# Optimization experiments

Hardware: AMD Instinct MI355X
Metric: run time of the kernel (lower is better)

## Reference

```python
import jax, jax.numpy as jnp
import numpy as np

LATENT = 64
HEADS = 4
N_A, N_B = 1024, 1024


def setup_inputs() -> dict:
    key = jax.random.key(0)
    ks = jax.random.split(key, 10)
    L = LATENT
    return {
        "rho_real": jax.random.normal(ks[0], (N_A, N_B), dtype=jnp.float32),
        "rho_imag": jax.random.normal(ks[1], (N_A, N_B), dtype=jnp.float32),
        "l_A": jax.random.randint(ks[2], (N_A,), 0, 3),
        "l_B": jax.random.randint(ks[3], (N_B,), 0, 3),
        "Z_A": 6,
        "Z_B": 8,
        # block_encoder: Linear(2, 64) -> SiLU -> Linear(64, latent_dim)
        "W1": jax.random.normal(ks[4], (64, 2), dtype=jnp.float32) * 0.5,
        "b1": jnp.zeros((64,), dtype=jnp.float32),
        "W2": jax.random.normal(ks[5], (L, 64), dtype=jnp.float32) * 0.1,
        "b2": jnp.zeros((L,), dtype=jnp.float32),
        # learned pooling query (1, latent_dim)
        "query": jax.random.normal(ks[6], (1, L), dtype=jnp.float32),
        # nn.MultiheadAttention packed in-projection and out-projection
        "in_proj_w": jax.random.normal(ks[7], (3 * L, L), dtype=jnp.float32) * 0.1,
        "in_proj_b": jnp.zeros((3 * L,), dtype=jnp.float32),
        "out_proj_w": jax.random.normal(ks[8], (L, L), dtype=jnp.float32) * 0.1,
        "out_proj_b": jnp.zeros((L,), dtype=jnp.float32),
    }


def reference(rho_real, rho_imag, l_A, l_B, Z_A, Z_B,
              W1, b1, W2, b2, query, in_proj_w, in_proj_b,
              out_proj_w, out_proj_b):
    L = query.shape[-1]
    H = HEADS
    hd = L // H
    # Batched equivalent of the per-(i,j) loop: all n_A*n_B elements at once.
    x = jnp.stack([rho_real.reshape(-1), rho_imag.reshape(-1)], axis=-1)  # [N, 2]
    h = jax.nn.silu(x @ W1.T + b1) @ W2.T + b2                            # [N, L]
    # MultiheadAttention with single query (batch=1, tgt_len=1, src_len=N)
    Wq, Wk, Wv = in_proj_w[:L], in_proj_w[L:2 * L], in_proj_w[2 * L:]
    bq, bk, bv = in_proj_b[:L], in_proj_b[L:2 * L], in_proj_b[2 * L:]
    q = (query @ Wq.T + bq).reshape(H, hd)        # [H, hd]
    k = (h @ Wk.T + bk).reshape(-1, H, hd)        # [N, H, hd]
    v = (h @ Wv.T + bv).reshape(-1, H, hd)        # [N, H, hd]
    scale = 1.0 / jnp.sqrt(jnp.asarray(hd, dtype=x.dtype))
    scores = jnp.einsum('hd,nhd->hn', q, k) * scale   # [H, N]
    attn = jax.nn.softmax(scores, axis=-1)
    pooled = jnp.einsum('hn,nhd->hd', attn, v).reshape(L)  # [L]
    return pooled @ out_proj_w.T + out_proj_b             # [latent_dim]
```

## Files before the change

### kernel.cpp

```cpp
#include <hip/hip_runtime.h>


#define LOG2E 1.44269504088896340736f
#define NLN2  (-0.69314718055994530942f)

#if __has_builtin(__builtin_amdgcn_exp2f)
#define EXP2(x) __builtin_amdgcn_exp2f(x)
#else
#define EXP2(x) exp2f(x)
#endif
#if __has_builtin(__builtin_amdgcn_rcpf)
#define RCP(x) __builtin_amdgcn_rcpf(x)
#else
#define RCP(x) (1.0f / (x))
#endif

#define LDS_WAIT() asm volatile("s_waitcnt lgkmcnt(0)" ::: "memory")

typedef __attribute__((ext_vector_type(8))) __bf16 bf16x8;
typedef __attribute__((ext_vector_type(4))) float  f32x4;
typedef __attribute__((ext_vector_type(2))) float  f32x2;

__device__ __forceinline__ f32x2 fma2(f32x2 a, f32x2 b, f32x2 c) {
#if __has_builtin(__builtin_elementwise_fma)
    return __builtin_elementwise_fma(a, b, c);
#else
    return (f32x2){fmaf(a.x, b.x, c.x), fmaf(a.y, b.y, c.y)};
#endif
}

#define WS_PK   0
#define WS_D    512
#define WS_ACC  768
#define NSLOT      16
#define SLOTSTRIDE 272

#define NPTS       (1024 * 1024)
#define K1_BLOCKS  2048
#define K1_THREADS 128
#define WAVES_TOTAL (K1_BLOCKS * 2)
#define GROUPS_PER_WAVE ((NPTS / 64) / WAVES_TOTAL)

#define PW_SHORTS  288
#define UW_SHORTS  (64 * 72)
#define WAVE_SHORTS (PW_SHORTS + UW_SHORTS)

__device__ __forceinline__ unsigned short to_bf16(float x) {
    return (unsigned short)((__float_as_uint(x) + 0x8000u) >> 16);
}

__global__ void setup_kernel(const float* __restrict__ W1, const float* __restrict__ b1,
                             const float* __restrict__ W2, const float* __restrict__ b2,
                             const float* __restrict__ query,
                             const float* __restrict__ ipw, const float* __restrict__ ipb,
                             float* __restrict__ ws)
{
    __shared__ float qv[64], qs[64], as4[4][64];
    const int t = threadIdx.x;
    const int b = blockIdx.x;

    for (int i = b * 64 + t; i < NSLOT * SLOTSTRIDE; i += 64 * 64)
        ws[WS_ACC + i] = 0.0f;

    qv[t] = query[t];
    __syncthreads();

    {
        float a = ipb[t];
        #pragma unroll
        for (int k = 0; k < 64; ++k) a = fmaf(ipw[t * 64 + k], qv[k], a);
        qs[t] = a;
    }
    __syncthreads();

    #pragma unroll
    for (int h = 0; h < 4; ++h) {
        float a = 0.0f;
        #pragma unroll
        for (int m = 0; m < 16; ++m)
            a = fmaf(ipw[(64 + h * 16 + m) * 64 + t], qs[h * 16 + m], a);
        as4[h][t] = 0.25f * a;
    }
    __syncthreads();

    const float w2 = W2[t * 64 + b];
    float g[4];
    #pragma unroll
    for (int h = 0; h < 4; ++h) {
        float v = as4[h][t] * w2;
        for (int m = 1; m < 64; m <<= 1) v += __shfl_xor(v, m);
        g[h] = v;
    }
    if (t == 0) {
        const int base = 16 * (b >> 1);
        const int sub  = b & 1;
        ws[WS_PK + base + 0  + sub] = -LOG2E * W1[2 * b];
        ws[WS_PK + base + 2  + sub] = -LOG2E * W1[2 * b + 1];
        ws[WS_PK + base + 4  + sub] = -LOG2E * b1[b];
        ws[WS_PK + base + 6  + sub] = 0.0f;
        ws[WS_PK + base + 8  + sub] = -g[0];
        ws[WS_PK + base + 10 + sub] = -g[1];
        ws[WS_PK + base + 12 + sub] = -g[2];
        ws[WS_PK + base + 14 + sub] = -g[3];
    }
    if (b == 0 && t < 4) {
        float d = 0.0f;
        #pragma unroll
        for (int c = 0; c < 64; ++c) d += as4[t][c] * b2[c];
        float qb = 0.0f;
        #pragma unroll
        for (int m = 0; m < 16; ++m) qb += qs[t * 16 + m] * ipb[64 + t * 16 + m];
        ws[WS_D + t] = LOG2E * (d + 0.25f * qb);
    }
}

__global__ __launch_bounds__(K1_THREADS) void main_kernel(
        const float* __restrict__ rr, const float* __restrict__ ri,
        const float4* __restrict__ pk4,
        const float* __restrict__ dvec, float* __restrict__ accb)
{
    __shared__ __align__(16) unsigned short lds[2][WAVE_SHORTS];

    const int t    = threadIdx.x;
    const int lane = t & 63;
    const int w    = t >> 6;
    const int m    = lane & 15;
    const int q    = lane >> 4;

    unsigned short* pw = lds[w];
    unsigned short* uw = lds[w] + PW_SHORTS;

    const float d0 = dvec[0], d1 = dvec[1], d2 = dvec[2], d3 = dvec[3];

    const int gwave = blockIdx.x * 2 + w;
    float l0 = 0, l1 = 0, l2 = 0, l3 = 0;
    f32x4 acc[4];
    #pragma unroll
    for (int i = 0; i < 4; ++i) acc[i] = (f32x4){0.f, 0.f, 0.f, 0.f};

    float rv[GROUPS_PER_WAVE], iv[GROUPS_PER_WAVE];
    #pragma unroll
    for (int it = 0; it < GROUPS_PER_WAVE; ++it) {
        const int idx = (gwave + it * WAVES_TOTAL) * 64 + lane;
        rv[it] = rr[idx];
        iv[it] = ri[idx];
    }

    for (int it = 0; it < GROUPS_PER_WAVE; ++it) {
        const f32x2 r2 = {rv[it], rv[it]};
        const f32x2 i2 = {iv[it], iv[it]};

        f32x2 s0v = {d0, 0.f}, s1v = {d1, 0.f}, s2v = {d2, 0.f}, s3v = {d3, 0.f};

        #pragma unroll 8
        for (int jp = 0; jp < 32; ++jp) {
            const float4 A  = pk4[4 * jp + 0];
            const float4 B  = pk4[4 * jp + 1];
            const float4 C  = pk4[4 * jp + 2];
            const float4 Dv = pk4[4 * jp + 3];

            const f32x2 cx = {A.x, A.y};
            const f32x2 cy = {A.z, A.w};
            const f32x2 cz = {B.x, B.y};

            const f32x2 zn = fma2(cx, r2, fma2(cy, i2, cz));
            const f32x2 e  = {EXP2(zn.x), EXP2(zn.y)};
            const f32x2 op = e + (f32x2){1.f, 1.f};
            const f32x2 rc = {RCP(op.x), RCP(op.y)};
            const f32x2 ub = zn * rc;

            s0v = fma2((f32x2){C.x,  C.y},  ub, s0v);
            s1v = fma2((f32x2){C.z,  C.w},  ub, s1v);
            s2v = fma2((f32x2){Dv.x, Dv.y}, ub, s2v);
            s3v = fma2((f32x2){Dv.z, Dv.w}, ub, s3v);

            uw[(2 * jp)     * 72 + lane] = to_bf16(ub.x);
            uw[(2 * jp + 1) * 72 + lane] = to_bf16(ub.y);
        }
        const float p0 = EXP2(s0v.x + s0v.y), p1 = EXP2(s1v.x + s1v.y);
        const float p2 = EXP2(s2v.x + s2v.y), p3 = EXP2(s3v.x + s3v.y);
        l0 += p0; l1 += p1; l2 += p2; l3 += p3;
        pw[0 * 72 + lane] = to_bf16(p0);
        pw[1 * 72 + lane] = to_bf16(p1);
        pw[2 * 72 + lane] = to_bf16(p2);
        pw[3 * 72 + lane] = to_bf16(p3);
        LDS_WAIT();

        const bf16x8 b0 = *(const bf16x8*)(pw + m * 72 + q * 8);
        const bf16x8 b1 = *(const bf16x8*)(pw + m * 72 + q * 8 + 32);
        #pragma unroll
        for (int tt = 0; tt < 4; ++tt) {
            const bf16x8 a0 = *(const bf16x8*)(uw + (16 * tt + m) * 72 + q * 8);
            const bf16x8 a1 = *(const bf16x8*)(uw + (16 * tt + m) * 72 + q * 8 + 32);
            acc[tt] = __builtin_amdgcn_mfma_f32_16x16x32_bf16(a0, b0, acc[tt], 0, 0, 0);
            acc[tt] = __builtin_amdgcn_mfma_f32_16x16x32_bf16(a1, b1, acc[tt], 0, 0, 0);
        }
        LDS_WAIT();
    }

    for (int mm = 1; mm < 64; mm <<= 1) {
        l0 += __shfl_xor(l0, mm);
        l1 += __shfl_xor(l1, mm);
        l2 += __shfl_xor(l2, mm);
        l3 += __shfl_xor(l3, mm);
    }

    float* scr = (float*)uw;
    if (m < 4) {
        #pragma unroll
        for (int tt = 0; tt < 4; ++tt)
            #pragma unroll
            for (int reg = 0; reg < 4; ++reg)
                scr[m * 66 + 16 * tt + 4 * q + reg] = acc[tt][reg];
    }
    LDS_WAIT();
    float Th[4];
    #pragma unroll
    for (int h = 0; h < 4; ++h) Th[h] = scr[h * 66 + lane];

    float* accS = accb + (blockIdx.x & (NSLOT - 1)) * SLOTSTRIDE;
    if (lane == 0) {
        atomicAdd(accS + 0, l0);
        atomicAdd(accS + 1, l1);
        atomicAdd(accS + 2, l2);
        atomicAdd(accS + 3, l3);
    }
    atomicAdd(accS + 4 + 0 * 64 + lane, Th[0]);
    atomicAdd(accS + 4 + 1 * 64 + lane, Th[1]);
    atomicAdd(accS + 4 + 2 * 64 + lane, Th[2]);
    atomicAdd(accS + 4 + 3 * 64 + lane, Th[3]);
}

__global__ void finish_kernel(const float* __restrict__ W2, const float* __restrict__ b2,
                              const float* __restrict__ ipw, const float* __restrict__ ipb,
                              const float* __restrict__ opw, const float* __restrict__ opb,
                              const float* __restrict__ ws, float* __restrict__ out)
{
    __shared__ float red[260];
    __shared__ float sb[256];
    __shared__ float pl[64];
    const int t = threadIdx.x;

    {
        float a = 0.0f;
        for (int s = 0; s < NSLOT; ++s) a += ws[WS_ACC + s * SLOTSTRIDE + t];
        red[t] = a;
        if (t < 4) {
            float a2 = 0.0f;
            for (int s = 0; s < NSLOT; ++s) a2 += ws[WS_ACC + s * SLOTSTRIDE + 256 + t];
            red[256 + t] = a2;
        }
    }
    __syncthreads();

    {
        const int h = t >> 6, j = t & 63;
        const float inv = NLN2 / red[h];
        float a = 0.0f;
        #pragma unroll
        for (int k = 0; k < 64; ++k) a += W2[j * 64 + k] * red[4 + h * 64 + k];
        sb[t] = fmaf(inv, a, b2[j]);
    }
    __syncthreads();

    if (t < 64) {
        const int h = t >> 4;
        float a = ipb[128 + t];
        #pragma unroll
        for (int d = 0; d < 64; ++d) a += ipw[(128 + t) * 64 + d] * sb[h * 64 + d];
        pl[t] = a;
    }
    __syncthreads();

    if (t < 64) {
        float a = opb[t];
        #pragma unroll
        for (int p = 0; p < 64; ++p) a += opw[t * 64 + p] * pl[p];
        out[t] = a;
    }
}

extern "C" void kernel_launch(void* const* d_in, const int* in_sizes, int n_in,
                              void* d_out, int out_size, void* d_ws, size_t ws_size,
                              hipStream_t stream)
{
    const float* rr  = (const float*)d_in[0];
    const float* ri  = (const float*)d_in[1];
    const float* W1  = (const float*)d_in[6];
    const float* b1  = (const float*)d_in[7];
    const float* W2  = (const float*)d_in[8];
    const float* b2  = (const float*)d_in[9];
    const float* qy  = (const float*)d_in[10];
    const float* ipw = (const float*)d_in[11];
    const float* ipb = (const float*)d_in[12];
    const float* opw = (const float*)d_in[13];
    const float* opb = (const float*)d_in[14];
    float* ws  = (float*)d_ws;
    float* out = (float*)d_out;

    setup_kernel<<<64, 64, 0, stream>>>(W1, b1, W2, b2, qy, ipw, ipb, ws);
    main_kernel<<<K1_BLOCKS, K1_THREADS, 0, stream>>>(
        rr, ri,
        (const float4*)(ws + WS_PK),
        ws + WS_D, ws + WS_ACC);
    finish_kernel<<<1, 256, 0, stream>>>(W2, b2, ipw, ipb, opw, opb, ws, out);
}
```

Baseline: 124.5 us.

## Fuse finish kernel into main kernel via last-block atomic counter

Removes the separate finish kernel launch. Each block of the main kernel now bumps a global counter, and the last block to arrive does the final reduction and projections in shared memory, reading the accumulators with agent-scope atomic loads. This saves one kernel launch and its gap, at the cost of a fence and atomic per block plus a serialized tail on a 128-thread block instead of 256 threads. It also adds a min-blocks-per-CU hint of 4 to launch_bounds.

```diff
diff --git a/kernel.cpp b/kernel.cpp
--- a/kernel.cpp
+++ b/kernel.cpp
@@ -29,11 +29,16 @@
 #endif
 }
 
+__device__ __forceinline__ float agent_load(const float* p) {
+    return __hip_atomic_load(p, __ATOMIC_RELAXED, __HIP_MEMORY_SCOPE_AGENT);
+}
+
 #define WS_PK   0
 #define WS_D    512
 #define WS_ACC  768
 #define NSLOT      16
 #define SLOTSTRIDE 272
+#define WS_CNT  (WS_ACC + NSLOT * SLOTSTRIDE)
 
 #define NPTS       (1024 * 1024)
 #define K1_BLOCKS  2048
@@ -59,7 +64,7 @@
     const int t = threadIdx.x;
     const int b = blockIdx.x;
 
-    for (int i = b * 64 + t; i < NSLOT * SLOTSTRIDE; i += 64 * 64)
+    for (int i = b * 64 + t; i < NSLOT * SLOTSTRIDE + 64; i += 64 * 64)
         ws[WS_ACC + i] = 0.0f;
 
     qv[t] = query[t];
@@ -114,12 +119,18 @@
     }
 }
 
-__global__ __launch_bounds__(K1_THREADS) void main_kernel(
+__global__ __launch_bounds__(K1_THREADS, 4) void main_kernel(
         const float* __restrict__ rr, const float* __restrict__ ri,
         const float4* __restrict__ pk4,
-        const float* __restrict__ dvec, float* __restrict__ accb)
+        const float* __restrict__ dvec, float* __restrict__ accb,
+        unsigned int* __restrict__ cnt,
+        const float* __restrict__ W2, const float* __restrict__ b2,
+        const float* __restrict__ ipw, const float* __restrict__ ipb,
+        const float* __restrict__ opw, const float* __restrict__ opb,
+        float* __restrict__ out)
 {
     __shared__ __align__(16) unsigned short lds[2][WAVE_SHORTS];
+    __shared__ unsigned int lastFlag;
 
     const int t    = threadIdx.x;
     const int lane = t & 63;
@@ -229,53 +240,53 @@
     atomicAdd(accS + 4 + 1 * 64 + lane, Th[1]);
     atomicAdd(accS + 4 + 2 * 64 + lane, Th[2]);
     atomicAdd(accS + 4 + 3 * 64 + lane, Th[3]);
-}
-
-__global__ void finish_kernel(const float* __restrict__ W2, const float* __restrict__ b2,
-                              const float* __restrict__ ipw, const float* __restrict__ ipb,
-                              const float* __restrict__ opw, const float* __restrict__ opb,
-                              const float* __restrict__ ws, float* __restrict__ out)
-{
-    __shared__ float red[260];
-    __shared__ float sb[256];
-    __shared__ float pl[64];
-    const int t = threadIdx.x;
-
-    {
+
+    __syncthreads();
+    if (t == 0) {
+        __threadfence();
+        const unsigned int prev =
+            __hip_atomic_fetch_add(cnt, 1u, __ATOMIC_ACQ_REL, __HIP_MEMORY_SCOPE_AGENT);
+        lastFlag = (prev == (unsigned int)(K1_BLOCKS - 1));
+    }
+    __syncthreads();
+    if (!lastFlag) return;
+
+    float* red = (float*)&lds[0][0];
+    float* sbv = red + 264;
+    float* plv = red + 520;
+
+    for (int i = t; i < 260; i += K1_THREADS) {
         float a = 0.0f;
-        for (int s = 0; s < NSLOT; ++s) a += ws[WS_ACC + s * SLOTSTRIDE + t];
-        red[t] = a;
-        if (t < 4) {
-            float a2 = 0.0f;
-            for (int s = 0; s < NSLOT; ++s) a2 += ws[WS_ACC + s * SLOTSTRIDE + 256 + t];
-            red[256 + t] = a2;
-        }
-    }
-    __syncthreads();
-
-    {
-        const int h = t >> 6, j = t & 63;
+        #pragma unroll
+        for (int s = 0; s < NSLOT; ++s)
+            a += agent_load(accb + s * SLOTSTRIDE + i);
+        red[i] = a;
+    }
+    __syncthreads();
+
+    for (int idx = t; idx < 256; idx += K1_THREADS) {
+        const int h = idx >> 6, j = idx & 63;
         const float inv = NLN2 / red[h];
         float a = 0.0f;
-        #pragma unroll
+        #pragma unroll 8
         for (int k = 0; k < 64; ++k) a += W2[j * 64 + k] * red[4 + h * 64 + k];
-        sb[t] = fmaf(inv, a, b2[j]);
+        sbv[idx] = fmaf(inv, a, b2[j]);
     }
     __syncthreads();
 
     if (t < 64) {
         const int h = t >> 4;
         float a = ipb[128 + t];
-        #pragma unroll
-        for (int d = 0; d < 64; ++d) a += ipw[(128 + t) * 64 + d] * sb[h * 64 + d];
-        pl[t] = a;
+        #pragma unroll 8
+        for (int d = 0; d < 64; ++d) a += ipw[(128 + t) * 64 + d] * sbv[h * 64 + d];
+        plv[t] = a;
     }
     __syncthreads();
 
     if (t < 64) {
         float a = opb[t];
-        #pragma unroll
-        for (int p = 0; p < 64; ++p) a += opw[t * 64 + p] * pl[p];
+        #pragma unroll 8
+        for (int p = 0; p < 64; ++p) a += opw[t * 64 + p] * plv[p];
         out[t] = a;
     }
 }
@@ -302,6 +313,7 @@
     main_kernel<<<K1_BLOCKS, K1_THREADS, 0, stream>>>(
         rr, ri,
         (const float4*)(ws + WS_PK),
-        ws + WS_D, ws + WS_ACC);
-    finish_kernel<<<1, 256, 0, stream>>>(W2, b2, ipw, ipb, opw, opb, ws, out);
-}
+        ws + WS_D, ws + WS_ACC,
+        (unsigned int*)(ws + WS_CNT),
+        W2, b2, ipw, ipb, opw, opb, out);
+}
```

New measurement: 174.6 us. 40.3% more time.
